# Optimization experiments

Measured on AMD Instinct MI355X. Metric: run time of the kernel, lower is better.

The kernel has to match this reference:

```python
import jax, jax.numpy as jnp
import numpy as np
from jax import lax

DIM, N_STATE, DT_RANK = 1024, 16, 64
BATCH, SEQ = 2, 2048


def setup_inputs() -> dict:
    key = jax.random.key(0)
    ks = jax.random.split(key, 12)
    s = 0.02
    x = jax.random.normal(ks[0], (BATCH, SEQ, DIM), dtype=jnp.float32)
    in_proj_w = jax.random.normal(ks[1], (2 * DIM, DIM), dtype=jnp.float32) * s
    conv_w = jax.random.normal(ks[2], (DIM, 1, 3), dtype=jnp.float32) * s
    conv_b = jax.random.normal(ks[3], (DIM,), dtype=jnp.float32) * s
    A_log = jax.random.normal(ks[4], (DIM, N_STATE), dtype=jnp.float32) * s
    D_param = jax.random.normal(ks[5], (DIM,), dtype=jnp.float32) * s
    x_proj_w = jax.random.normal(ks[6], (DT_RANK + 2 * N_STATE, DIM), dtype=jnp.float32) * s
    # dt_proj init mimics the torch module: bias = inv-softplus of dt in [dt_min, dt_max]
    dt = jnp.exp(jax.random.uniform(ks[7], (DIM,)) * (np.log(0.1) - np.log(0.001)) + np.log(0.001))
    dt = jnp.clip(dt, 0.0001, None)
    inv_dt = dt + jnp.log(-jnp.expm1(-dt))
    dt_init_std = DT_RANK ** (-0.5)
    dt_proj_w = jnp.tile(inv_dt[:, None], (1, DT_RANK)) * dt_init_std
    dt_proj_b = inv_dt
    out_proj_w = jax.random.normal(ks[8], (DIM, DIM), dtype=jnp.float32) * s
    return {
        "x": x, "in_proj_w": in_proj_w, "conv_w": conv_w, "conv_b": conv_b,
        "A_log": A_log, "D_param": D_param, "x_proj_w": x_proj_w,
        "dt_proj_w": dt_proj_w, "dt_proj_b": dt_proj_b, "out_proj_w": out_proj_w,
    }


def _selective_scan(u, delta, A, Bp, Cp, D_param):
    # u, delta: (B, L, D); A: (D, N); Bp, Cp: (B, L, N)
    deltaA = jnp.exp(delta[..., None] * A)                       # (B, L, D, N)
    deltaB_u = delta[..., None] * Bp[:, :, None, :] * u[..., None]  # (B, L, D, N)

    def step(state, inputs):
        dA_t, dBu_t, C_t = inputs          # (B, D, N), (B, D, N), (B, N)
        state = dA_t * state + dBu_t       # (B, D, N)
        y_t = jnp.einsum("bdn,bn->bd", state, C_t)
        return state, y_t

    init = jnp.zeros((u.shape[0], u.shape[2], A.shape[1]), dtype=u.dtype)
    xs = (jnp.swapaxes(deltaA, 0, 1), jnp.swapaxes(deltaB_u, 0, 1), jnp.swapaxes(Cp, 0, 1))
    _, ys = lax.scan(step, init, xs)       # ys: (L, B, D)
    y = jnp.swapaxes(ys, 0, 1)             # (B, L, D)
    return y + u * D_param


def reference(x, in_proj_w, conv_w, conv_b, A_log, D_param, x_proj_w, dt_proj_w, dt_proj_b, out_proj_w):
    B, L, D = x.shape
    xz = x @ in_proj_w.T                   # (B, L, 2D)
    xc, z = jnp.split(xz, 2, axis=-1)
    # depthwise conv1d, kernel 3, padding 1 (output length == L)
    xc = jnp.swapaxes(xc, 1, 2)            # (B, D, L)
    xc = lax.conv_general_dilated(
        xc, conv_w, window_strides=(1,), padding=[(1, 1)],
        dimension_numbers=("NCH", "OIH", "NCH"), feature_group_count=D,
    ) + conv_b[None, :, None]
    xc = jnp.swapaxes(xc, 1, 2)            # (B, L, D)
    x_dbl = xc @ x_proj_w.T                # (B, L, dt_rank + 2N)
    dt_r, Bp, Cp = jnp.split(x_dbl, [DT_RANK, DT_RANK + N_STATE], axis=-1)
    delta = jax.nn.softplus(dt_r @ dt_proj_w.T + dt_proj_b)   # (B, L, D)
    A = -jnp.exp(A_log)                    # (D, N)
    y = _selective_scan(xc, delta, A, Bp, Cp, D_param)
    y = y * jax.nn.silu(z)
    return y @ out_proj_w.T
```

## Files before the change

### kernel.cpp

```cpp
#include <hip/hip_runtime.h>
#include <math.h>

#define BATCH 2
#define SEQ   2048
#define DIM   1024
#define NST   16
#define DTR   64
#define KSL   8

typedef _Float16 f16x8 __attribute__((ext_vector_type(8)));
typedef float f32x4 __attribute__((ext_vector_type(4)));

__device__ __forceinline__ float softplus_f(float v) {
  return fmaxf(v, 0.f) + log1pf(expf(-fabsf(v)));
}

__device__ __forceinline__ void gl_lds16(const _Float16* g, _Float16* l) {
  __builtin_amdgcn_global_load_lds(
      (const __attribute__((address_space(1))) void*)g,
      (__attribute__((address_space(3))) void*)l, 16, 0, 0);
}

#define FMA_ROW(i, av)                                        \
  acc[i][0] = fmaf(av, b.x, acc[i][0]);                       \
  acc[i][1] = fmaf(av, b.y, acc[i][1]);                       \
  acc[i][2] = fmaf(av, b.z, acc[i][2]);                       \
  acc[i][3] = fmaf(av, b.w, acc[i][3]);

__global__ __launch_bounds__(256) void k_cvt3(
    const float* __restrict__ in0, _Float16* __restrict__ hi0,
    _Float16* __restrict__ lo0,
    const float* __restrict__ in1, _Float16* __restrict__ hi1,
    _Float16* __restrict__ lo1,
    const float* __restrict__ in2, _Float16* __restrict__ hi2,
    _Float16* __restrict__ lo2) {
  int bb = blockIdx.x;
  const float* in;
  _Float16 *hi, *lo;
  if (bb < 2048) {
    in = in0; hi = hi0; lo = lo0;
  } else if (bb < 3072) {
    in = in1; hi = hi1; lo = lo1; bb -= 2048;
  } else {
    in = in2; hi = hi2; lo = lo2; bb -= 3072;
  }
  const int i = (bb * 256 + threadIdx.x) * 8;
  const float4 a = *(const float4*)(in + i);
  const float4 b = *(const float4*)(in + i + 4);
  const float v[8] = {a.x, a.y, a.z, a.w, b.x, b.y, b.z, b.w};
  f16x8 h, l;
#pragma unroll
  for (int j = 0; j < 8; ++j) {
    const _Float16 hh = (_Float16)v[j];
    h[j] = hh;
    l[j] = (_Float16)(v[j] - (float)hh);
  }
  *(f16x8*)(hi + i) = h;
  *(f16x8*)(lo + i) = l;
}

template <int EPI>
__global__ __launch_bounds__(256) void kgemm_f16x3(
    const _Float16* __restrict__ Ah, const _Float16* __restrict__ Al,
    const _Float16* __restrict__ Bh, const _Float16* __restrict__ Bl,
    float* __restrict__ out0, float* __restrict__ out1) {
  __shared__ _Float16 sm[32768];
  const int tid = threadIdx.x;
  const int wid = tid >> 6, lane = tid & 63;
  const int wm = wid >> 1, wn = wid & 1;
  const int m0 = blockIdx.y * 128;
  const int n0 = blockIdx.x * 128;

  const int r0 = wid * 32;
  const int srow = lane >> 2;
  const int skqs = ((lane & 3) ^ ((lane >> 3) & 3)) * 8;
  const _Float16* gAh = Ah + (size_t)(m0 + r0 + srow) * 1024 + skqs;
  const _Float16* gAl = Al + (size_t)(m0 + r0 + srow) * 1024 + skqs;
  const _Float16* gBh = Bh + (size_t)(n0 + r0 + srow) * 1024 + skqs;
  const _Float16* gBl = Bl + (size_t)(n0 + r0 + srow) * 1024 + skqs;

  const int fr = lane & 15;
  const int fks = (((lane >> 4) ^ ((fr >> 1) & 3))) * 8;

  f32x4 acc[4][4];
#pragma unroll
  for (int i = 0; i < 4; ++i)
#pragma unroll
    for (int j = 0; j < 4; ++j) acc[i][j] = (f32x4)(0.f);

  auto STAGE = [&](int buf, int k0) {
    _Float16* base = sm + buf * 16384;
    _Float16* lA = base + r0 * 32;
    gl_lds16(gAh + k0, lA);
    gl_lds16(gAh + k0 + 16 * 1024, lA + 512);
    gl_lds16(gAl + k0, lA + 4096);
    gl_lds16(gAl + k0 + 16 * 1024, lA + 4096 + 512);
    gl_lds16(gBh + k0, lA + 8192);
    gl_lds16(gBh + k0 + 16 * 1024, lA + 8192 + 512);
    gl_lds16(gBl + k0, lA + 12288);
    gl_lds16(gBl + k0 + 16 * 1024, lA + 12288 + 512);
  };

  STAGE(0, 0);
  int cur = 0;
  for (int k0 = 0; k0 < 1024; k0 += 32) {
    __syncthreads();
    if (k0 + 32 < 1024) STAGE(cur ^ 1, k0 + 32);
    const _Float16* base = sm + cur * 16384;

    f16x8 ah[4], alo[4], bh[4], blo[4];
#pragma unroll
    for (int i = 0; i < 4; ++i) {
      const int ao = (wm * 64 + i * 16 + fr) * 32 + fks;
      const int bo = (wn * 64 + i * 16 + fr) * 32 + fks;
      ah[i]  = *(const f16x8*)(base + ao);
      alo[i] = *(const f16x8*)(base + 4096 + ao);
      bh[i]  = *(const f16x8*)(base + 8192 + bo);
      blo[i] = *(const f16x8*)(base + 12288 + bo);
    }
#pragma unroll
    for (int i = 0; i < 4; ++i)
#pragma unroll
      for (int j = 0; j < 4; ++j) {
        acc[i][j] = __builtin_amdgcn_mfma_f32_16x16x32_f16(ah[i], bh[j],
                                                           acc[i][j], 0, 0, 0);
        acc[i][j] = __builtin_amdgcn_mfma_f32_16x16x32_f16(ah[i], blo[j],
                                                           acc[i][j], 0, 0, 0);
        acc[i][j] = __builtin_amdgcn_mfma_f32_16x16x32_f16(alo[i], bh[j],
                                                           acc[i][j], 0, 0, 0);
      }
    cur ^= 1;
  }

  const int lr4 = (lane >> 4) * 4, lc = lane & 15;
#pragma unroll
  for (int i = 0; i < 4; ++i) {
#pragma unroll
    for (int j = 0; j < 4; ++j) {
      const int ar = m0 + wm * 64 + i * 16 + lr4;
      const int bc = n0 + wn * 64 + j * 16 + lc;
#pragma unroll
      for (int r = 0; r < 4; ++r) {
        const float v = acc[i][j][r];
        if (EPI == 0) {
          out0[(size_t)(ar + r) * 1024 + bc] = v;
        } else {
          const int bb = bc >> 11, tt = bc & 2047;
          if (ar < 1024) {
            out0[((size_t)bb * 1024 + ar + r) * 2048 + tt] = v;
          } else {
            out1[((size_t)bb * 1024 + (ar + r - 1024)) * 2048 + tt] = v;
          }
        }
      }
    }
  }
}

__global__ __launch_bounds__(256) void k_conv(
    const float* __restrict__ xcraw, const float* __restrict__ cw,
    const float* __restrict__ cb, float* __restrict__ xc) {
  const int idx = blockIdx.x * 256 + threadIdx.x;
  const int t0 = (idx & (SEQ / 4 - 1)) * 4;
  const int r = idx >> 9;
  const int d = r & (DIM - 1);
  const float w0 = cw[d * 3 + 0], w1 = cw[d * 3 + 1], w2 = cw[d * 3 + 2];
  const float bias = cb[d];
  const float* in = xcraw + (size_t)r * SEQ;
  float o[4];
#pragma unroll
  for (int j = 0; j < 4; ++j) {
    const int t = t0 + j;
    const float xm = (t > 0) ? in[t - 1] : 0.f;
    const float x0 = in[t];
    const float xp = (t < SEQ - 1) ? in[t + 1] : 0.f;
    o[j] = fmaf(w0, xm, fmaf(w1, x0, fmaf(w2, xp, bias)));
  }
  *(float4*)(xc + (size_t)r * SEQ + t0) = make_float4(o[0], o[1], o[2], o[3]);
}

__global__ __launch_bounds__(256) void k2_xproj_sk(
    const float* __restrict__ xc, const float* __restrict__ wp,
    float* __restrict__ part) {
  __shared__ float As[16][100];
  __shared__ float Bs[16][132];
  const int tid = threadIdx.x;
  const int tile = blockIdx.x;
  const int ks = blockIdx.y;
  const int b = tile >> 4;
  const int t0 = (tile & 15) * 128;
  const int kbase = ks * (DIM / KSL);
  const int tx = tid & 15, ty = tid >> 4;
  float acc[6][8] = {{0.f}};
  for (int k = 0; k < DIM / KSL; k += 16) {
    float a_reg[6];
#pragma unroll
    for (int i = 0; i < 6; ++i) {
      const int ii = tid + 256 * i;
      a_reg[i] = wp[(size_t)(ii >> 4) * DIM + kbase + k + (ii & 15)];
    }
    float4 b_reg[2];
#pragma unroll
    for (int r = 0; r < 2; ++r) {
      const int id2 = tid + 256 * r;
      const int krow = id2 >> 5, t4 = (id2 & 31) * 4;
      b_reg[r] = *(const float4*)(xc + ((size_t)b * DIM + kbase + k + krow) *
                                           SEQ + t0 + t4);
    }
    __syncthreads();
#pragma unroll
    for (int i = 0; i < 6; ++i) {
      const int ii = tid + 256 * i;
      As[ii & 15][ii >> 4] = a_reg[i];
    }
#pragma unroll
    for (int r = 0; r < 2; ++r) {
      const int id2 = tid + 256 * r;
      const int krow = id2 >> 5, t4 = (id2 & 31) * 4;
      *(float4*)&Bs[krow][t4] = b_reg[r];
    }
    __syncthreads();
#pragma unroll
    for (int kk = 0; kk < 16; ++kk) {
      const float4 bA = *(const float4*)&Bs[kk][tx * 4];
      const float4 bB = *(const float4*)&Bs[kk][64 + tx * 4];
#pragma unroll
      for (int i = 0; i < 6; ++i) {
        const float a = As[kk][ty + 16 * i];
        acc[i][0] = fmaf(a, bA.x, acc[i][0]);
        acc[i][1] = fmaf(a, bA.y, acc[i][1]);
        acc[i][2] = fmaf(a, bA.z, acc[i][2]);
        acc[i][3] = fmaf(a, bA.w, acc[i][3]);
        acc[i][4] = fmaf(a, bB.x, acc[i][4]);
        acc[i][5] = fmaf(a, bB.y, acc[i][5]);
        acc[i][6] = fmaf(a, bB.z, acc[i][6]);
        acc[i][7] = fmaf(a, bB.w, acc[i][7]);
      }
    }
    __syncthreads();
  }
#pragma unroll
  for (int i = 0; i < 6; ++i) {
    const int j = ty + 16 * i;
    const size_t o = ((size_t)(ks * BATCH + b) * 96 + j) * SEQ + t0;
    *(float4*)(part + o + tx * 4) =
        make_float4(acc[i][0], acc[i][1], acc[i][2], acc[i][3]);
    *(float4*)(part + o + 64 + tx * 4) =
        make_float4(acc[i][4], acc[i][5], acc[i][6], acc[i][7]);
  }
}

__global__ __launch_bounds__(256) void k_red(const float* __restrict__ part,
                                             float* __restrict__ xdbl) {
  const size_t PL = (size_t)BATCH * 96 * SEQ;
  const size_t i4 = ((size_t)blockIdx.x * 256 + threadIdx.x) * 4;
  float4 s = *(const float4*)(part + i4);
#pragma unroll
  for (int ks = 1; ks < KSL; ++ks) {
    const float4 v = *(const float4*)(part + ks * PL + i4);
    s.x += v.x; s.y += v.y; s.z += v.z; s.w += v.w;
  }
  *(float4*)(xdbl + i4) = s;
}

__global__ __launch_bounds__(256) void k3_dtproj(
    const float* __restrict__ xdbl, const float* __restrict__ dtw,
    const float* __restrict__ dtb, float* __restrict__ delta) {
  __shared__ float As[16][68];
  __shared__ float Bs[16][68];
  const int tid = threadIdx.x;
  const int b = blockIdx.z;
  const int d0 = blockIdx.y * 64;
  const int t0 = blockIdx.x * 64;
  const int tx = tid & 15, ty = tid >> 4;
  const int lrow = tid >> 2, lcol = (tid & 3) * 4;
  const int bk = tid >> 4, bt4 = (tid & 15) * 4;
  float acc[4][4] = {{0.f}};
  for (int k = 0; k < DTR; k += 16) {
    const float4 av =
        *(const float4*)(dtw + (size_t)(d0 + lrow) * DTR + k + lcol);
    const float4 bv =
        *(const float4*)(xdbl + ((size_t)b * 96 + k + bk) * SEQ + t0 + bt4);
    __syncthreads();
    As[lcol + 0][lrow] = av.x; As[lcol + 1][lrow] = av.y;
    As[lcol + 2][lrow] = av.z; As[lcol + 3][lrow] = av.w;
    Bs[bk][bt4 + 0] = bv.x; Bs[bk][bt4 + 1] = bv.y;
    Bs[bk][bt4 + 2] = bv.z; Bs[bk][bt4 + 3] = bv.w;
    __syncthreads();
#pragma unroll
    for (int kk = 0; kk < 16; ++kk) {
      const float4 a = *(const float4*)&As[kk][ty * 4];
      const float4 b = *(const float4*)&Bs[kk][tx * 4];
      FMA_ROW(0, a.x) FMA_ROW(1, a.y) FMA_ROW(2, a.z) FMA_ROW(3, a.w)
    }
  }
#pragma unroll
  for (int i = 0; i < 4; ++i) {
    const int d = d0 + ty * 4 + i;
    const float bias = dtb[d];
    float4 v;
    v.x = softplus_f(acc[i][0] + bias);
    v.y = softplus_f(acc[i][1] + bias);
    v.z = softplus_f(acc[i][2] + bias);
    v.w = softplus_f(acc[i][3] + bias);
    *(float4*)(delta + ((size_t)b * DIM + d) * SEQ + t0 + tx * 4) = v;
  }
}

__global__ __launch_bounds__(1024) void k_scan_fused(
    const float* __restrict__ delta, const float* __restrict__ u,
    const float* __restrict__ xdbl, const float* __restrict__ A_log,
    const float* __restrict__ Dp, const float* __restrict__ z,
    float* __restrict__ y) {
  __shared__ float red[2][NST][2][260];
  const int tid = threadIdx.x;
  const int wv = tid >> 6;
  const int lane = tid & 63;
  const int idx = blockIdx.x;
  const int b = idx >> 10, d = idx & (DIM - 1);
  const float A = -expf(A_log[d * NST + wv]);
  const float Dprm = Dp[d];
  const float* drow = delta + (size_t)idx * SEQ;
  const float* urow = u + (size_t)idx * SEQ;
  const float* Brow = xdbl + ((size_t)b * 96 + DTR + wv) * SEQ;
  const float* Crow = xdbl + ((size_t)b * 96 + DTR + NST + wv) * SEQ;
  const float* zrow = z + (size_t)idx * SEQ;
  float* yrow = y + (size_t)idx * SEQ;
  float s_c = 0.f;
  const int tl = lane * 8;
  const int tl2 = lane * 4;

  float4 dA = *(const float4*)(drow + tl);
  float4 dB = *(const float4*)(drow + tl + 4);
  float4 uA = *(const float4*)(urow + tl);
  float4 uB = *(const float4*)(urow + tl + 4);
  float4 bA = *(const float4*)(Brow + tl);
  float4 bB = *(const float4*)(Brow + tl + 4);

  for (int w = 0; w < SEQ / 512; ++w) {
    const int t0 = w * 512;
    const float4 cA = *(const float4*)(Crow + t0 + tl);
    const float4 cB = *(const float4*)(Crow + t0 + tl + 4);
    float p[8], q[8];
    {
      const float dls[8] = {dA.x, dA.y, dA.z, dA.w, dB.x, dB.y, dB.z, dB.w};
      const float us[8]  = {uA.x, uA.y, uA.z, uA.w, uB.x, uB.y, uB.z, uB.w};
      const float Bb[8]  = {bA.x, bA.y, bA.z, bA.w, bB.x, bB.y, bB.z, bB.w};
      p[0] = __expf(dls[0] * A);
      q[0] = dls[0] * us[0] * Bb[0];
#pragma unroll
      for (int i = 1; i < 8; ++i) {
        const float a = __expf(dls[i] * A);
        const float bq = dls[i] * us[i] * Bb[i];
        p[i] = a * p[i - 1];
        q[i] = fmaf(a, q[i - 1], bq);
      }
    }
    if (w + 1 < SEQ / 512) {
      const int tn = t0 + 512 + tl;
      dA = *(const float4*)(drow + tn);
      dB = *(const float4*)(drow + tn + 4);
      uA = *(const float4*)(urow + tn);
      uB = *(const float4*)(urow + tn + 4);
      bA = *(const float4*)(Brow + tn);
      bB = *(const float4*)(Brow + tn + 4);
    }
    float ia = p[7], ib = q[7];
#pragma unroll
    for (int sft = 1; sft < 64; sft <<= 1) {
      const float oa = __shfl_up(ia, sft, 64);
      const float ob = __shfl_up(ib, sft, 64);
      if (lane >= sft) { ib = fmaf(ia, ob, ib); ia = ia * oa; }
    }
    const float Wa = __shfl(ia, 63, 64);
    const float Wb = __shfl(ib, 63, 64);
    float ea = __shfl_up(ia, 1, 64);
    float eb = __shfl_up(ib, 1, 64);
    if (lane == 0) { ea = 1.f; eb = 0.f; }
    const float S = fmaf(ea, s_c, eb);
    s_c = fmaf(Wa, s_c, Wb);
    float4 y0, y1;
    y0.x = fmaf(p[0], S, q[0]) * cA.x;
    y0.y = fmaf(p[1], S, q[1]) * cA.y;
    y0.z = fmaf(p[2], S, q[2]) * cA.z;
    y0.w = fmaf(p[3], S, q[3]) * cA.w;
    y1.x = fmaf(p[4], S, q[4]) * cB.x;
    y1.y = fmaf(p[5], S, q[5]) * cB.y;
    y1.z = fmaf(p[6], S, q[6]) * cB.z;
    y1.w = fmaf(p[7], S, q[7]) * cB.w;
    *(float4*)&red[w & 1][wv][0][tl2] = y0;
    *(float4*)&red[w & 1][wv][1][tl2] = y1;
    __syncthreads();
    if (tid < 512) {
      const int sub = (tid >> 2) & 1;
      const int pos = ((tid >> 3) << 2) | (tid & 3);
      float sum = 0.f;
#pragma unroll
      for (int nn = 0; nn < NST; ++nn) sum += red[w & 1][nn][sub][pos];
      const float uD = urow[t0 + tid];
      sum = fmaf(uD, Dprm, sum);
      const float zz = zrow[t0 + tid];
      const float sg = __builtin_amdgcn_rcpf(1.f + __expf(-zz));
      yrow[t0 + tid] = sum * zz * sg;
    }
  }
}

__global__ __launch_bounds__(256) void k_gt(
    const float* __restrict__ y, _Float16* __restrict__ gh,
    _Float16* __restrict__ gl) {
  __shared__ _Float16 th[64][68];
  __shared__ _Float16 tl[64][68];
  const int ti = threadIdx.x;
  const int t0 = blockIdx.x * 64;
  const int d0 = blockIdx.y * 64;
  const int b = blockIdx.z;
  const int c4 = (ti & 15) * 4;
#pragma unroll
  for (int rr = 0; rr < 4; ++rr) {
    const int dl_ = (ti >> 4) + 16 * rr;
    const size_t base = ((size_t)b * DIM + d0 + dl_) * SEQ + t0 + c4;
    const float4 yv = *(const float4*)(y + base);
    const float gy[4] = {yv.x, yv.y, yv.z, yv.w};
#pragma unroll
    for (int k = 0; k < 4; ++k) {
      const _Float16 h = (_Float16)gy[k];
      th[dl_][c4 + k] = h;
      tl[dl_][c4 + k] = (_Float16)(gy[k] - (float)h);
    }
  }
  __syncthreads();
#pragma unroll
  for (int rr = 0; rr < 2; ++rr) {
    const int chunk = ti + 256 * rr;
    const int tloc = chunk >> 3;
    const int dchunk = (chunk & 7) * 8;
    f16x8 hv, lv;
#pragma unroll
    for (int j = 0; j < 8; ++j) {
      hv[j] = th[dchunk + j][tloc];
      lv[j] = tl[dchunk + j][tloc];
    }
    const size_t o = ((size_t)b * SEQ + t0 + tloc) * DIM + d0 + dchunk;
    *(f16x8*)(gh + o) = hv;
    *(f16x8*)(gl + o) = lv;
  }
}

extern "C" void kernel_launch(void* const* d_in, const int* in_sizes, int n_in,
                              void* d_out, int out_size, void* d_ws,
                              size_t ws_size, hipStream_t stream) {
  const float* x          = (const float*)d_in[0];
  const float* in_proj_w  = (const float*)d_in[1];
  const float* conv_w     = (const float*)d_in[2];
  const float* conv_b     = (const float*)d_in[3];
  const float* A_log      = (const float*)d_in[4];
  const float* D_param    = (const float*)d_in[5];
  const float* x_proj_w   = (const float*)d_in[6];
  const float* dt_proj_w  = (const float*)d_in[7];
  const float* dt_proj_b  = (const float*)d_in[8];
  const float* out_proj_w = (const float*)d_in[9];
  float* out = (float*)d_out;
  float* ws = (float*)d_ws;

  const size_t PLANE = (size_t)BATCH * SEQ * DIM;
  float* xcraw = ws;
  float* delta = ws;
  _Float16* gh = (_Float16*)ws;
  _Float16* gl = (_Float16*)ws + PLANE;
  float* xc    = ws + PLANE;
  float* zbuf  = ws + 2 * PLANE;
  _Float16* xh = (_Float16*)(ws + 3 * PLANE);
  _Float16* xl = xh + PLANE;
  float* part  = ws + 3 * PLANE;
  float* ybuf  = ws + 3 * PLANE;
  float* xdbl  = ws + 4 * PLANE;
  _Float16* wih = (_Float16*)(ws + 4 * PLANE + 1572864);
  _Float16* wil = wih + (size_t)2 * DIM * DIM;
  _Float16* woh = wil + (size_t)2 * DIM * DIM;
  _Float16* wol = woh + (size_t)DIM * DIM;

  k_cvt3<<<dim3(3584), 256, 0, stream>>>(x, xh, xl, in_proj_w, wih, wil,
                                         out_proj_w, woh, wol);

  kgemm_f16x3<1><<<dim3(32, 16), 256, 0, stream>>>(wih, wil, xh, xl,
                                                   xcraw, zbuf);
  k_conv<<<dim3((BATCH * DIM * SEQ / 4) / 256), 256, 0, stream>>>(
      xcraw, conv_w, conv_b, xc);
  k2_xproj_sk<<<dim3(32, KSL), 256, 0, stream>>>(xc, x_proj_w, part);
  k_red<<<dim3(384), 256, 0, stream>>>(part, xdbl);
  k3_dtproj<<<dim3(SEQ / 64, DIM / 64, BATCH), 256, 0, stream>>>(
      xdbl, dt_proj_w, dt_proj_b, delta);
  k_scan_fused<<<dim3(BATCH * DIM), 1024, 0, stream>>>(
      delta, xc, xdbl, A_log, D_param, zbuf, ybuf);
  k_gt<<<dim3(SEQ / 64, DIM / 64, BATCH), 256, 0, stream>>>(ybuf, gh, gl);
  kgemm_f16x3<0><<<dim3(8, 32), 256, 0, stream>>>(gh, gl, woh, wol,
                                                  out, nullptr);
}
```

Measured before the change: 302.4 us.

## Restructure scan to one 32-step chunk per lane with single cross-lane prefix

The scan kernel now gives each lane a contiguous 32-timestep chunk covering the whole sequence, instead of looping over four 512-step windows that each need a wave prefix scan and a carried state. It first computes the chunk's composite (a,b) transform, runs one wave-level shuffle scan, then replays the chunk sequentially to produce outputs. The outputs go into a swizzled LDS buffer and are reduced over states in two halves, and all 1024 threads now do the reduce instead of 512. This cuts the number of shuffle scans and barriers. In exchange it recomputes the exponentials in the second pass, reads delta, u and B twice, and the strided per-lane global loads may coalesce worse.

```diff
diff --git a/kernel.cpp b/kernel.cpp
--- a/kernel.cpp
+++ b/kernel.cpp
@@ -312,7 +312,7 @@
     const float* __restrict__ xdbl, const float* __restrict__ A_log,
     const float* __restrict__ Dp, const float* __restrict__ z,
     float* __restrict__ y) {
-  __shared__ float red[2][NST][2][260];
+  __shared__ float red[NST][1024];
   const int tid = threadIdx.x;
   const int wv = tid >> 6;
   const int lane = tid & 63;
@@ -326,83 +326,93 @@
   const float* Crow = xdbl + ((size_t)b * 96 + DTR + NST + wv) * SEQ;
   const float* zrow = z + (size_t)idx * SEQ;
   float* yrow = y + (size_t)idx * SEQ;
-  float s_c = 0.f;
-  const int tl = lane * 8;
-  const int tl2 = lane * 4;
-
-  float4 dA = *(const float4*)(drow + tl);
-  float4 dB = *(const float4*)(drow + tl + 4);
-  float4 uA = *(const float4*)(urow + tl);
-  float4 uB = *(const float4*)(urow + tl + 4);
-  float4 bA = *(const float4*)(Brow + tl);
-  float4 bB = *(const float4*)(Brow + tl + 4);
-
-  for (int w = 0; w < SEQ / 512; ++w) {
-    const int t0 = w * 512;
-    const float4 cA = *(const float4*)(Crow + t0 + tl);
-    const float4 cB = *(const float4*)(Crow + t0 + tl + 4);
-    float p[8], q[8];
+
+  const int rl = tid >> 4, re = tid & 15;
+  const int tR0 = rl * 32 + re;
+  const int tR1 = rl * 32 + 16 + re;
+  const float uR0 = urow[tR0], uR1 = urow[tR1];
+  const float zR0 = zrow[tR0], zR1 = zrow[tR1];
+
+  const int tb = lane * 32;
+
+  float Pa = 1.f, Pb = 0.f;
+#pragma unroll
+  for (int c = 0; c < 8; ++c) {
+    const float4 d4 = *(const float4*)(drow + tb + c * 4);
+    const float4 u4 = *(const float4*)(urow + tb + c * 4);
+    const float4 B4 = *(const float4*)(Brow + tb + c * 4);
+    const float dd[4] = {d4.x, d4.y, d4.z, d4.w};
+    const float uu[4] = {u4.x, u4.y, u4.z, u4.w};
+    const float BB[4] = {B4.x, B4.y, B4.z, B4.w};
+#pragma unroll
+    for (int j = 0; j < 4; ++j) {
+      const float a = __expf(dd[j] * A);
+      const float bq = dd[j] * uu[j] * BB[j];
+      Pb = fmaf(a, Pb, bq);
+      Pa *= a;
+    }
+  }
+
+  float ia = Pa, ib = Pb;
+#pragma unroll
+  for (int sft = 1; sft < 64; sft <<= 1) {
+    const float oa = __shfl_up(ia, sft, 64);
+    const float ob = __shfl_up(ib, sft, 64);
+    if (lane >= sft) { ib = fmaf(ia, ob, ib); ia = ia * oa; }
+  }
+  float S = __shfl_up(ib, 1, 64);
+  if (lane == 0) S = 0.f;
+
+  float s = S;
+  const int swz = (lane >> 1) & 3;
+  float* myrow = &red[wv][lane * 16];
+  const int rc = re >> 2, rj = re & 3;
+  const int roff = rl * 16 + (((rc + ((rl >> 1) & 3)) & 3) * 4) + rj;
+
+#pragma unroll
+  for (int h = 0; h < 2; ++h) {
+#pragma unroll
+    for (int c = 0; c < 4; ++c) {
+      const int t = tb + h * 16 + c * 4;
+      const float4 d4 = *(const float4*)(drow + t);
+      const float4 u4 = *(const float4*)(urow + t);
+      const float4 B4 = *(const float4*)(Brow + t);
+      const float4 C4 = *(const float4*)(Crow + t);
+      float4 yv;
+      {
+        const float a = __expf(d4.x * A);
+        s = fmaf(a, s, d4.x * u4.x * B4.x);
+        yv.x = s * C4.x;
+      }
+      {
+        const float a = __expf(d4.y * A);
+        s = fmaf(a, s, d4.y * u4.y * B4.y);
+        yv.y = s * C4.y;
+      }
+      {
+        const float a = __expf(d4.z * A);
+        s = fmaf(a, s, d4.z * u4.z * B4.z);
+        yv.z = s * C4.z;
+      }
+      {
+        const float a = __expf(d4.w * A);
+        s = fmaf(a, s, d4.w * u4.w * B4.w);
+        yv.w = s * C4.w;
+      }
+      *(float4*)&myrow[((c + swz) & 3) * 4] = yv;
+    }
+    __syncthreads();
     {
-      const float dls[8] = {dA.x, dA.y, dA.z, dA.w, dB.x, dB.y, dB.z, dB.w};
-      const float us[8]  = {uA.x, uA.y, uA.z, uA.w, uB.x, uB.y, uB.z, uB.w};
-      const float Bb[8]  = {bA.x, bA.y, bA.z, bA.w, bB.x, bB.y, bB.z, bB.w};
-      p[0] = __expf(dls[0] * A);
-      q[0] = dls[0] * us[0] * Bb[0];
-#pragma unroll
-      for (int i = 1; i < 8; ++i) {
-        const float a = __expf(dls[i] * A);
-        const float bq = dls[i] * us[i] * Bb[i];
-        p[i] = a * p[i - 1];
-        q[i] = fmaf(a, q[i - 1], bq);
-      }
-    }
-    if (w + 1 < SEQ / 512) {
-      const int tn = t0 + 512 + tl;
-      dA = *(const float4*)(drow + tn);
-      dB = *(const float4*)(drow + tn + 4);
-      uA = *(const float4*)(urow + tn);
-      uB = *(const float4*)(urow + tn + 4);
-      bA = *(const float4*)(Brow + tn);
-      bB = *(const float4*)(Brow + tn + 4);
-    }
-    float ia = p[7], ib = q[7];
-#pragma unroll
-    for (int sft = 1; sft < 64; sft <<= 1) {
-      const float oa = __shfl_up(ia, sft, 64);
-      const float ob = __shfl_up(ib, sft, 64);
-      if (lane >= sft) { ib = fmaf(ia, ob, ib); ia = ia * oa; }
-    }
-    const float Wa = __shfl(ia, 63, 64);
-    const float Wb = __shfl(ib, 63, 64);
-    float ea = __shfl_up(ia, 1, 64);
-    float eb = __shfl_up(ib, 1, 64);
-    if (lane == 0) { ea = 1.f; eb = 0.f; }
-    const float S = fmaf(ea, s_c, eb);
-    s_c = fmaf(Wa, s_c, Wb);
-    float4 y0, y1;
-    y0.x = fmaf(p[0], S, q[0]) * cA.x;
-    y0.y = fmaf(p[1], S, q[1]) * cA.y;
-    y0.z = fmaf(p[2], S, q[2]) * cA.z;
-    y0.w = fmaf(p[3], S, q[3]) * cA.w;
-    y1.x = fmaf(p[4], S, q[4]) * cB.x;
-    y1.y = fmaf(p[5], S, q[5]) * cB.y;
-    y1.z = fmaf(p[6], S, q[6]) * cB.z;
-    y1.w = fmaf(p[7], S, q[7]) * cB.w;
-    *(float4*)&red[w & 1][wv][0][tl2] = y0;
-    *(float4*)&red[w & 1][wv][1][tl2] = y1;
-    __syncthreads();
-    if (tid < 512) {
-      const int sub = (tid >> 2) & 1;
-      const int pos = ((tid >> 3) << 2) | (tid & 3);
       float sum = 0.f;
 #pragma unroll
-      for (int nn = 0; nn < NST; ++nn) sum += red[w & 1][nn][sub][pos];
-      const float uD = urow[t0 + tid];
+      for (int nn = 0; nn < NST; ++nn) sum += red[nn][roff];
+      const float uD = h ? uR1 : uR0;
+      const float zz = h ? zR1 : zR0;
       sum = fmaf(uD, Dprm, sum);
-      const float zz = zrow[t0 + tid];
       const float sg = __builtin_amdgcn_rcpf(1.f + __expf(-zz));
-      yrow[t0 + tid] = sum * zz * sg;
-    }
+      yrow[h ? tR1 : tR0] = sum * zz * sg;
+    }
+    if (h == 0) __syncthreads();
   }
 }
 
```

New measurement: 720.3 us. +138.2%, slower.

## Restructure scan into batched wave prefix pass then recompute pass

Applied to the files above, without the earlier changes.

The selective-scan kernel now computes per-lane segment aggregates for all four 512-step windows first and runs the 64-lane shuffle prefix scan on all four at once. This exposes instruction-level parallelism across windows and removes the serial dependence between each window's scan. A second pass reloads delta/u/B, recomputes the exponentials, and produces outputs sequentially from the prefix state. It also preloads u and z for the epilogue into registers. The trade-off is doubled global reads of delta, u and B and doubled exp work, plus higher register pressure.

```diff
diff --git a/kernel.cpp b/kernel.cpp
--- a/kernel.cpp
+++ b/kernel.cpp
@@ -326,82 +326,165 @@
   const float* Crow = xdbl + ((size_t)b * 96 + DTR + NST + wv) * SEQ;
   const float* zrow = z + (size_t)idx * SEQ;
   float* yrow = y + (size_t)idx * SEQ;
-  float s_c = 0.f;
   const int tl = lane * 8;
   const int tl2 = lane * 4;
 
-  float4 dA = *(const float4*)(drow + tl);
-  float4 dB = *(const float4*)(drow + tl + 4);
-  float4 uA = *(const float4*)(urow + tl);
-  float4 uB = *(const float4*)(urow + tl + 4);
-  float4 bA = *(const float4*)(Brow + tl);
-  float4 bB = *(const float4*)(Brow + tl + 4);
-
-  for (int w = 0; w < SEQ / 512; ++w) {
-    const int t0 = w * 512;
-    const float4 cA = *(const float4*)(Crow + t0 + tl);
-    const float4 cB = *(const float4*)(Crow + t0 + tl + 4);
-    float p[8], q[8];
-    {
+  float uR[4], zR[4];
+  if (tid < 512) {
+#pragma unroll
+    for (int w = 0; w < 4; ++w) {
+      uR[w] = urow[w * 512 + tid];
+      zR[w] = zrow[w * 512 + tid];
+    }
+  }
+
+  float ia[4], ib[4];
+  {
+    float4 dA = *(const float4*)(drow + tl);
+    float4 dB = *(const float4*)(drow + tl + 4);
+    float4 uA = *(const float4*)(urow + tl);
+    float4 uB = *(const float4*)(urow + tl + 4);
+    float4 bA = *(const float4*)(Brow + tl);
+    float4 bB = *(const float4*)(Brow + tl + 4);
+#pragma unroll
+    for (int w = 0; w < 4; ++w) {
       const float dls[8] = {dA.x, dA.y, dA.z, dA.w, dB.x, dB.y, dB.z, dB.w};
       const float us[8]  = {uA.x, uA.y, uA.z, uA.w, uB.x, uB.y, uB.z, uB.w};
       const float Bb[8]  = {bA.x, bA.y, bA.z, bA.w, bB.x, bB.y, bB.z, bB.w};
-      p[0] = __expf(dls[0] * A);
-      q[0] = dls[0] * us[0] * Bb[0];
+      if (w < 3) {
+        const int tn = (w + 1) * 512 + tl;
+        dA = *(const float4*)(drow + tn);
+        dB = *(const float4*)(drow + tn + 4);
+        uA = *(const float4*)(urow + tn);
+        uB = *(const float4*)(urow + tn + 4);
+        bA = *(const float4*)(Brow + tn);
+        bB = *(const float4*)(Brow + tn + 4);
+      }
+      float Pa, Pb;
+      Pa = __expf(dls[0] * A);
+      Pb = dls[0] * us[0] * Bb[0];
 #pragma unroll
       for (int i = 1; i < 8; ++i) {
         const float a = __expf(dls[i] * A);
-        const float bq = dls[i] * us[i] * Bb[i];
-        p[i] = a * p[i - 1];
-        q[i] = fmaf(a, q[i - 1], bq);
-      }
-    }
-    if (w + 1 < SEQ / 512) {
-      const int tn = t0 + 512 + tl;
-      dA = *(const float4*)(drow + tn);
-      dB = *(const float4*)(drow + tn + 4);
-      uA = *(const float4*)(urow + tn);
-      uB = *(const float4*)(urow + tn + 4);
-      bA = *(const float4*)(Brow + tn);
-      bB = *(const float4*)(Brow + tn + 4);
-    }
-    float ia = p[7], ib = q[7];
-#pragma unroll
-    for (int sft = 1; sft < 64; sft <<= 1) {
-      const float oa = __shfl_up(ia, sft, 64);
-      const float ob = __shfl_up(ib, sft, 64);
-      if (lane >= sft) { ib = fmaf(ia, ob, ib); ia = ia * oa; }
-    }
-    const float Wa = __shfl(ia, 63, 64);
-    const float Wb = __shfl(ib, 63, 64);
-    float ea = __shfl_up(ia, 1, 64);
-    float eb = __shfl_up(ib, 1, 64);
-    if (lane == 0) { ea = 1.f; eb = 0.f; }
-    const float S = fmaf(ea, s_c, eb);
-    s_c = fmaf(Wa, s_c, Wb);
-    float4 y0, y1;
-    y0.x = fmaf(p[0], S, q[0]) * cA.x;
-    y0.y = fmaf(p[1], S, q[1]) * cA.y;
-    y0.z = fmaf(p[2], S, q[2]) * cA.z;
-    y0.w = fmaf(p[3], S, q[3]) * cA.w;
-    y1.x = fmaf(p[4], S, q[4]) * cB.x;
-    y1.y = fmaf(p[5], S, q[5]) * cB.y;
-    y1.z = fmaf(p[6], S, q[6]) * cB.z;
-    y1.w = fmaf(p[7], S, q[7]) * cB.w;
-    *(float4*)&red[w & 1][wv][0][tl2] = y0;
-    *(float4*)&red[w & 1][wv][1][tl2] = y1;
-    __syncthreads();
-    if (tid < 512) {
-      const int sub = (tid >> 2) & 1;
-      const int pos = ((tid >> 3) << 2) | (tid & 3);
-      float sum = 0.f;
-#pragma unroll
-      for (int nn = 0; nn < NST; ++nn) sum += red[w & 1][nn][sub][pos];
-      const float uD = urow[t0 + tid];
-      sum = fmaf(uD, Dprm, sum);
-      const float zz = zrow[t0 + tid];
-      const float sg = __builtin_amdgcn_rcpf(1.f + __expf(-zz));
-      yrow[t0 + tid] = sum * zz * sg;
+        Pb = fmaf(a, Pb, dls[i] * us[i] * Bb[i]);
+        Pa *= a;
+      }
+      ia[w] = Pa;
+      ib[w] = Pb;
+    }
+  }
+
+#pragma unroll
+  for (int sft = 1; sft < 64; sft <<= 1) {
+    float oa[4], ob[4];
+#pragma unroll
+    for (int w = 0; w < 4; ++w) {
+      oa[w] = __shfl_up(ia[w], sft, 64);
+      ob[w] = __shfl_up(ib[w], sft, 64);
+    }
+    if (lane >= sft) {
+#pragma unroll
+      for (int w = 0; w < 4; ++w) {
+        ib[w] = fmaf(ia[w], ob[w], ib[w]);
+        ia[w] = ia[w] * oa[w];
+      }
+    }
+  }
+  float S[4];
+  {
+    float sc = 0.f;
+#pragma unroll
+    for (int w = 0; w < 4; ++w) {
+      const float Wa = __shfl(ia[w], 63, 64);
+      const float Wb = __shfl(ib[w], 63, 64);
+      float ea = __shfl_up(ia[w], 1, 64);
+      float eb = __shfl_up(ib[w], 1, 64);
+      if (lane == 0) { ea = 1.f; eb = 0.f; }
+      S[w] = fmaf(ea, sc, eb);
+      sc = fmaf(Wa, sc, Wb);
+    }
+  }
+
+  {
+    float4 dA = *(const float4*)(drow + tl);
+    float4 dB = *(const float4*)(drow + tl + 4);
+    float4 uA = *(const float4*)(urow + tl);
+    float4 uB = *(const float4*)(urow + tl + 4);
+    float4 bA = *(const float4*)(Brow + tl);
+    float4 bB = *(const float4*)(Brow + tl + 4);
+#pragma unroll
+    for (int w = 0; w < 4; ++w) {
+      const int t0 = w * 512;
+      const float4 cA = *(const float4*)(Crow + t0 + tl);
+      const float4 cB = *(const float4*)(Crow + t0 + tl + 4);
+      const float dls[8] = {dA.x, dA.y, dA.z, dA.w, dB.x, dB.y, dB.z, dB.w};
+      const float us[8]  = {uA.x, uA.y, uA.z, uA.w, uB.x, uB.y, uB.z, uB.w};
+      const float Bb[8]  = {bA.x, bA.y, bA.z, bA.w, bB.x, bB.y, bB.z, bB.w};
+      if (w < 3) {
+        const int tn = (w + 1) * 512 + tl;
+        dA = *(const float4*)(drow + tn);
+        dB = *(const float4*)(drow + tn + 4);
+        uA = *(const float4*)(urow + tn);
+        uB = *(const float4*)(urow + tn + 4);
+        bA = *(const float4*)(Brow + tn);
+        bB = *(const float4*)(Brow + tn + 4);
+      }
+      float s = S[w];
+      float4 y0, y1;
+      {
+        const float a = __expf(dls[0] * A);
+        s = fmaf(a, s, dls[0] * us[0] * Bb[0]);
+        y0.x = s * cA.x;
+      }
+      {
+        const float a = __expf(dls[1] * A);
+        s = fmaf(a, s, dls[1] * us[1] * Bb[1]);
+        y0.y = s * cA.y;
+      }
+      {
+        const float a = __expf(dls[2] * A);
+        s = fmaf(a, s, dls[2] * us[2] * Bb[2]);
+        y0.z = s * cA.z;
+      }
+      {
+        const float a = __expf(dls[3] * A);
+        s = fmaf(a, s, dls[3] * us[3] * Bb[3]);
+        y0.w = s * cA.w;
+      }
+      {
+        const float a = __expf(dls[4] * A);
+        s = fmaf(a, s, dls[4] * us[4] * Bb[4]);
+        y1.x = s * cB.x;
+      }
+      {
+        const float a = __expf(dls[5] * A);
+        s = fmaf(a, s, dls[5] * us[5] * Bb[5]);
+        y1.y = s * cB.y;
+      }
+      {
+        const float a = __expf(dls[6] * A);
+        s = fmaf(a, s, dls[6] * us[6] * Bb[6]);
+        y1.z = s * cB.z;
+      }
+      {
+        const float a = __expf(dls[7] * A);
+        s = fmaf(a, s, dls[7] * us[7] * Bb[7]);
+        y1.w = s * cB.w;
+      }
+      *(float4*)&red[w & 1][wv][0][tl2] = y0;
+      *(float4*)&red[w & 1][wv][1][tl2] = y1;
+      __syncthreads();
+      if (tid < 512) {
+        const int sub = (tid >> 2) & 1;
+        const int pos = ((tid >> 3) << 2) | (tid & 3);
+        float sum = 0.f;
+#pragma unroll
+        for (int nn = 0; nn < NST; ++nn) sum += red[w & 1][nn][sub][pos];
+        sum = fmaf(uR[w], Dprm, sum);
+        const float zz = zR[w];
+        const float sg = __builtin_amdgcn_rcpf(1.f + __expf(-zz));
+        yrow[t0 + tid] = sum * zz * sg;
+      }
     }
   }
 }
```

Measured after the change: 324.5 us. +7.3%, slower.
